# Optimization experiments

Hardware: AMD Instinct MI355X
Metric: run time of the kernel (lower is better)

Reference implementation:

```python
import jax, jax.numpy as jnp
import numpy as np

BS, H, L, D = 16, 16, 4096, 32  # bs, n_heads, seq_len(=q_len), head_dim

def setup_inputs() -> dict:
    key = jax.random.key(0)
    kq, kk, kv = jax.random.split(key, 3)
    q = jax.random.normal(kq, (BS, H, L, D), dtype=jnp.float32)
    k = jax.random.normal(kk, (BS, H, D, L), dtype=jnp.float32)
    v = jax.random.normal(kv, (BS, H, L, D), dtype=jnp.float32)
    return {"q": q, "k": k, "v": v}

def reference(q, k, v):
    # reordered attention: scores = (k @ v) / sqrt(seq_len) -> [bs,h,d_k,d_v]
    seq_len = v.shape[2]
    scores = jnp.einsum('bhds,bhse->bhde', k, v) / jnp.sqrt(jnp.float32(seq_len))
    # faithful to source: softmax over dim=0 (the batch dimension)
    attn_weights = jax.nn.softmax(scores, axis=0)
    # dropout p=0.0 -> identity
    # output = q @ weights -> [bs,h,q_len,d_v]
    output = jnp.einsum('bhld,bhde->bhle', q, attn_weights)
    return output, attn_weights
```

## Files before the change

### kernel.cpp

```cpp
#include <hip/hip_runtime.h>

#define BS 16
#define NH 16
#define LQ 4096
#define DH 32

constexpr int SPLIT = 8;
constexpr int SCHUNK = LQ / SPLIT;
constexpr size_t OUT_ELEMS = (size_t)BS * NH * LQ * DH;
constexpr int HDE = NH * DH * DH;

__device__ __forceinline__ void async_cp16(float* dst, const float* src) {
    __builtin_amdgcn_global_load_lds(
        (const __attribute__((address_space(1))) void*)src,
        (__attribute__((address_space(3))) void*)dst, 16, 0, 0);
}

__device__ __forceinline__ void fma4(float4& a, float s, const float4& v) {
    a.x = fmaf(s, v.x, a.x);
    a.y = fmaf(s, v.y, a.y);
    a.z = fmaf(s, v.z, a.z);
    a.w = fmaf(s, v.w, a.w);
}

__global__ __launch_bounds__(256, 2) void kv_partial(const float* __restrict__ k,
                                                     const float* __restrict__ v,
                                                     float* __restrict__ part) {
    __shared__ float lds[16384];
    const int tid  = threadIdx.x;
    const int wid  = tid >> 6;
    const int lane = tid & 63;
    const int p    = blockIdx.x & (SPLIT - 1);
    const int bh   = blockIdx.x >> 3;

    const int dgl = lane >> 3;
    const int d0  = dgl << 2;
    const int e0  = (lane & 7) << 2;

    const float* kb = k + (size_t)bh * DH * LQ;
    const float* vb = v + (size_t)bh * LQ * DH;
    const int s_blk = p * SCHUNK;

    float* kt = lds;
    float* vt = lds + 8192;

    float4 acc0 = {0,0,0,0}, acc1 = {0,0,0,0}, acc2 = {0,0,0,0}, acc3 = {0,0,0,0};

#pragma unroll
    for (int st = 0; st < 2; ++st) {
        const int sb = s_blk + (st << 8);

#pragma unroll
        for (int i = 0; i < 8; ++i) {
            const int d = (wid << 3) + i;
            async_cp16(kt + (d << 8),
                       kb + (size_t)d * LQ + sb + ((lane ^ (d >> 2)) << 2));
            const int o = (((wid << 3) + i) << 8);
            async_cp16(vt + o, vb + (((size_t)sb) << 5) + o + (lane << 2));
        }
        __syncthreads();

#pragma unroll 4
        for (int gg = 0; gg < 16; ++gg) {
            const int g  = (wid << 4) + gg;
            const int ko = (g ^ dgl) << 2;
            const float4 kq0 = *(const float4*)(kt + ((d0 + 0) << 8) + ko);
            const float4 kq1 = *(const float4*)(kt + ((d0 + 1) << 8) + ko);
            const float4 kq2 = *(const float4*)(kt + ((d0 + 2) << 8) + ko);
            const float4 kq3 = *(const float4*)(kt + ((d0 + 3) << 8) + ko);
            const int vo = (g << 7) + e0;
            const float4 vv0 = *(const float4*)(vt + vo);
            const float4 vv1 = *(const float4*)(vt + vo + 32);
            const float4 vv2 = *(const float4*)(vt + vo + 64);
            const float4 vv3 = *(const float4*)(vt + vo + 96);

            fma4(acc0, kq0.x, vv0); fma4(acc0, kq0.y, vv1); fma4(acc0, kq0.z, vv2); fma4(acc0, kq0.w, vv3);
            fma4(acc1, kq1.x, vv0); fma4(acc1, kq1.y, vv1); fma4(acc1, kq1.z, vv2); fma4(acc1, kq1.w, vv3);
            fma4(acc2, kq2.x, vv0); fma4(acc2, kq2.y, vv1); fma4(acc2, kq2.z, vv2); fma4(acc2, kq2.w, vv3);
            fma4(acc3, kq3.x, vv0); fma4(acc3, kq3.y, vv1); fma4(acc3, kq3.z, vv2); fma4(acc3, kq3.w, vv3);
        }
        __syncthreads();
    }

    float* red = lds;
    *(float4*)(red + (wid << 10) + ((d0 + 0) << 5) + e0) = acc0;
    *(float4*)(red + (wid << 10) + ((d0 + 1) << 5) + e0) = acc1;
    *(float4*)(red + (wid << 10) + ((d0 + 2) << 5) + e0) = acc2;
    *(float4*)(red + (wid << 10) + ((d0 + 3) << 5) + e0) = acc3;
    __syncthreads();

    const int t4 = tid << 2;
    const float4 r0 = *(const float4*)(red + t4);
    const float4 r1 = *(const float4*)(red + 1024 + t4);
    const float4 r2 = *(const float4*)(red + 2048 + t4);
    const float4 r3 = *(const float4*)(red + 3072 + t4);
    float4 r;
    r.x = (r0.x + r1.x) + (r2.x + r3.x);
    r.y = (r0.y + r1.y) + (r2.y + r3.y);
    r.z = (r0.z + r1.z) + (r2.z + r3.z);
    r.w = (r0.w + r1.w) + (r2.w + r3.w);
    *(float4*)(part + ((size_t)p * (BS * NH) + bh) * 1024 + t4) = r;
}

__global__ __launch_bounds__(256) void softmax_b(const float* __restrict__ part,
                                                 float* __restrict__ wts) {
    int idx = blockIdx.x * 256 + threadIdx.x;

    float sc[BS];
#pragma unroll
    for (int b = 0; b < BS; ++b) {
        float s = 0.f;
#pragma unroll
        for (int pp = 0; pp < SPLIT; ++pp) {
            s += part[(((size_t)pp * BS * NH + (size_t)b * NH) << 10) + idx];
        }
        sc[b] = s * (1.0f / 64.0f);
    }

    float m = sc[0];
#pragma unroll
    for (int b = 1; b < BS; ++b) m = fmaxf(m, sc[b]);
    float sum = 0.f;
#pragma unroll
    for (int b = 0; b < BS; ++b) { sc[b] = __expf(sc[b] - m); sum += sc[b]; }
    float inv = 1.0f / sum;
#pragma unroll
    for (int b = 0; b < BS; ++b) {
        wts[(size_t)b * HDE + idx] = sc[b] * inv;
    }
}

__global__ __launch_bounds__(256, 2) void qw(const float* __restrict__ q,
                                             const float* __restrict__ wts,
                                             float* __restrict__ out) {
    __shared__ float qs[128 * 36];
    const int blk = blockIdx.x;
    const int bh  = blk >> 5;
    const int lt  = blk & 31;
    const int tid = threadIdx.x;

    const float* qbase = q + ((size_t)bh * LQ + lt * 128) * DH;

#pragma unroll
    for (int pp = 0; pp < 4; ++pp) {
        const int idx = pp * 256 + tid;
        const int row = idx >> 3;
        const int c4  = idx & 7;
        const float4 t = *(const float4*)(qbase + idx * 4);
        *(float4*)(qs + row * 36 + c4 * 4) = t;
    }

    const int lsub = tid >> 3;
    const int e0   = (tid & 7) << 2;

    float4 Wf[32];
    const float* wbase = wts + (size_t)bh * (DH * DH) + e0;
#pragma unroll
    for (int d = 0; d < 32; ++d) Wf[d] = *(const float4*)(wbase + d * DH);

    __syncthreads();

    float* obase = out + ((size_t)bh * LQ + lt * 128) * DH;

#pragma unroll
    for (int r = 0; r < 4; ++r) {
        const int lr = lsub + r * 32;
        const float* qrow = qs + lr * 36;
        float4 acc = {0,0,0,0};
#pragma unroll
        for (int d4 = 0; d4 < 32; d4 += 4) {
            const float4 qv = *(const float4*)(qrow + d4);
            fma4(acc, qv.x, Wf[d4 + 0]);
            fma4(acc, qv.y, Wf[d4 + 1]);
            fma4(acc, qv.z, Wf[d4 + 2]);
            fma4(acc, qv.w, Wf[d4 + 3]);
        }
        *(float4*)(obase + (size_t)lr * DH + e0) = acc;
    }
}

extern "C" void kernel_launch(void* const* d_in, const int* in_sizes, int n_in,
                              void* d_out, int out_size, void* d_ws, size_t ws_size,
                              hipStream_t stream) {
    const float* q = (const float*)d_in[0];
    const float* k = (const float*)d_in[1];
    const float* v = (const float*)d_in[2];
    float* out  = (float*)d_out;
    float* wts  = out + OUT_ELEMS;
    float* part = (float*)d_ws;

    kv_partial<<<BS * NH * SPLIT, 256, 0, stream>>>(k, v, part);
    softmax_b<<<HDE / 256, 256, 0, stream>>>(part, wts);
    qw<<<BS * NH * (LQ / 128), 256, 0, stream>>>(q, wts, out);
}
```

Measured before the change: 160.2 us.

## Make kv_partial waves independent with register-prefetched double buffering in private LDS

Each wave of kv_partial now owns a private LDS slice and a contiguous 128-element sequence range. It prefetches K and V tiles into registers while computing on the current tile, which replaces the block-wide async global-to-LDS copies and __syncthreads barriers. LDS use is halved and launch bounds are raised to four blocks per CU to increase occupancy. The risks are higher register pressure, and correctness now relies on wave-local ordering enforced with s_waitcnt instead of barriers.

Measured after the change: 217.0 us. 35.4% more time.

```diff
diff --git a/kernel.cpp b/kernel.cpp
--- a/kernel.cpp
+++ b/kernel.cpp
@@ -9,12 +9,6 @@
 constexpr int SCHUNK = LQ / SPLIT;
 constexpr size_t OUT_ELEMS = (size_t)BS * NH * LQ * DH;
 constexpr int HDE = NH * DH * DH;
-
-__device__ __forceinline__ void async_cp16(float* dst, const float* src) {
-    __builtin_amdgcn_global_load_lds(
-        (const __attribute__((address_space(1))) void*)src,
-        (__attribute__((address_space(3))) void*)dst, 16, 0, 0);
-}
 
 __device__ __forceinline__ void fma4(float4& a, float s, const float4& v) {
     a.x = fmaf(s, v.x, a.x);
@@ -23,10 +17,10 @@
     a.w = fmaf(s, v.w, a.w);
 }
 
-__global__ __launch_bounds__(256, 2) void kv_partial(const float* __restrict__ k,
+__global__ __launch_bounds__(256, 4) void kv_partial(const float* __restrict__ k,
                                                      const float* __restrict__ v,
                                                      float* __restrict__ part) {
-    __shared__ float lds[16384];
+    __shared__ float lds[8192];
     const int tid  = threadIdx.x;
     const int wid  = tid >> 6;
     const int lane = tid & 63;
@@ -39,61 +33,76 @@
 
     const float* kb = k + (size_t)bh * DH * LQ;
     const float* vb = v + (size_t)bh * LQ * DH;
-    const int s_blk = p * SCHUNK;
-
-    float* kt = lds;
-    float* vt = lds + 8192;
+    const int s_wave = p * SCHUNK + (wid << 7);
+
+    float* kw = lds + (wid << 11);
+    float* vw = kw + 1024;
+
+    const int kd = lane >> 1;
+    const float* kg = kb + (size_t)kd * LQ + s_wave + ((lane & 1) << 4);
+    const float* vg = vb + ((size_t)s_wave << 5) + (lane << 2);
+
+    int kst[4];
+#pragma unroll
+    for (int j = 0; j < 4; ++j)
+        kst[j] = (kd << 5) + ((((((lane & 1) << 2) | j) ^ (kd >> 2)) & 7) << 2);
+
+    float4 kr[4], vr[4];
+#pragma unroll
+    for (int j = 0; j < 4; ++j) kr[j] = *(const float4*)(kg + (j << 2));
+#pragma unroll
+    for (int i = 0; i < 4; ++i) vr[i] = *(const float4*)(vg + (i << 8));
 
     float4 acc0 = {0,0,0,0}, acc1 = {0,0,0,0}, acc2 = {0,0,0,0}, acc3 = {0,0,0,0};
 
-#pragma unroll
-    for (int st = 0; st < 2; ++st) {
-        const int sb = s_blk + (st << 8);
-
-#pragma unroll
-        for (int i = 0; i < 8; ++i) {
-            const int d = (wid << 3) + i;
-            async_cp16(kt + (d << 8),
-                       kb + (size_t)d * LQ + sb + ((lane ^ (d >> 2)) << 2));
-            const int o = (((wid << 3) + i) << 8);
-            async_cp16(vt + o, vb + (((size_t)sb) << 5) + o + (lane << 2));
-        }
-        __syncthreads();
-
-#pragma unroll 4
-        for (int gg = 0; gg < 16; ++gg) {
-            const int g  = (wid << 4) + gg;
-            const int ko = (g ^ dgl) << 2;
-            const float4 kq0 = *(const float4*)(kt + ((d0 + 0) << 8) + ko);
-            const float4 kq1 = *(const float4*)(kt + ((d0 + 1) << 8) + ko);
-            const float4 kq2 = *(const float4*)(kt + ((d0 + 2) << 8) + ko);
-            const float4 kq3 = *(const float4*)(kt + ((d0 + 3) << 8) + ko);
+#pragma unroll 1
+    for (int t = 0; t < 4; ++t) {
+        asm volatile("s_waitcnt lgkmcnt(0)" ::: "memory");
+#pragma unroll
+        for (int j = 0; j < 4; ++j) *(float4*)(kw + kst[j]) = kr[j];
+#pragma unroll
+        for (int i = 0; i < 4; ++i) *(float4*)(vw + (i << 8) + (lane << 2)) = vr[i];
+
+        if (t < 3) {
+            const int so = (t + 1) << 5;
+#pragma unroll
+            for (int j = 0; j < 4; ++j) kr[j] = *(const float4*)(kg + so + (j << 2));
+#pragma unroll
+            for (int i = 0; i < 4; ++i) vr[i] = *(const float4*)(vg + ((size_t)so << 5) + (i << 8));
+        }
+
+#pragma unroll
+        for (int g = 0; g < 8; ++g) {
+            const int ko = (d0 << 5) + ((g ^ dgl) << 2);
+            const float4 kq0 = *(const float4*)(kw + ko);
+            const float4 kq1 = *(const float4*)(kw + ko + 32);
+            const float4 kq2 = *(const float4*)(kw + ko + 64);
+            const float4 kq3 = *(const float4*)(kw + ko + 96);
             const int vo = (g << 7) + e0;
-            const float4 vv0 = *(const float4*)(vt + vo);
-            const float4 vv1 = *(const float4*)(vt + vo + 32);
-            const float4 vv2 = *(const float4*)(vt + vo + 64);
-            const float4 vv3 = *(const float4*)(vt + vo + 96);
+            const float4 vv0 = *(const float4*)(vw + vo);
+            const float4 vv1 = *(const float4*)(vw + vo + 32);
+            const float4 vv2 = *(const float4*)(vw + vo + 64);
+            const float4 vv3 = *(const float4*)(vw + vo + 96);
 
             fma4(acc0, kq0.x, vv0); fma4(acc0, kq0.y, vv1); fma4(acc0, kq0.z, vv2); fma4(acc0, kq0.w, vv3);
             fma4(acc1, kq1.x, vv0); fma4(acc1, kq1.y, vv1); fma4(acc1, kq1.z, vv2); fma4(acc1, kq1.w, vv3);
             fma4(acc2, kq2.x, vv0); fma4(acc2, kq2.y, vv1); fma4(acc2, kq2.z, vv2); fma4(acc2, kq2.w, vv3);
             fma4(acc3, kq3.x, vv0); fma4(acc3, kq3.y, vv1); fma4(acc3, kq3.z, vv2); fma4(acc3, kq3.w, vv3);
         }
-        __syncthreads();
-    }
-
-    float* red = lds;
-    *(float4*)(red + (wid << 10) + ((d0 + 0) << 5) + e0) = acc0;
-    *(float4*)(red + (wid << 10) + ((d0 + 1) << 5) + e0) = acc1;
-    *(float4*)(red + (wid << 10) + ((d0 + 2) << 5) + e0) = acc2;
-    *(float4*)(red + (wid << 10) + ((d0 + 3) << 5) + e0) = acc3;
+    }
+
+    asm volatile("s_waitcnt lgkmcnt(0)" ::: "memory");
+    *(float4*)(kw + ((d0 + 0) << 5) + e0) = acc0;
+    *(float4*)(kw + ((d0 + 1) << 5) + e0) = acc1;
+    *(float4*)(kw + ((d0 + 2) << 5) + e0) = acc2;
+    *(float4*)(kw + ((d0 + 3) << 5) + e0) = acc3;
     __syncthreads();
 
     const int t4 = tid << 2;
-    const float4 r0 = *(const float4*)(red + t4);
-    const float4 r1 = *(const float4*)(red + 1024 + t4);
-    const float4 r2 = *(const float4*)(red + 2048 + t4);
-    const float4 r3 = *(const float4*)(red + 3072 + t4);
+    const float4 r0 = *(const float4*)(lds + t4);
+    const float4 r1 = *(const float4*)(lds + 2048 + t4);
+    const float4 r2 = *(const float4*)(lds + 4096 + t4);
+    const float4 r3 = *(const float4*)(lds + 6144 + t4);
     float4 r;
     r.x = (r0.x + r1.x) + (r2.x + r3.x);
     r.y = (r0.y + r1.y) + (r2.y + r3.y);
```

## Split KV reduction into finer sequence chunks with separate partial-sum reduce kernel

Applied to the files above, without the earlier changes.

The K·V partial kernel now works on 128-wide sequence chunks with half the LDS and a higher occupancy hint. When the workspace is large enough it launches 32 splits per (b,h) instead of 8, which raises the block count. The partial sums are reduced in a new fully parallel kernel that writes scaled scores into the weights buffer, and the softmax then runs in place. The cost is more partial-sum traffic and one extra kernel launch.

Result: faster. 146.0 us (-8.9%).

```diff
diff --git a/kernel.cpp b/kernel.cpp
--- a/kernel.cpp
+++ b/kernel.cpp
@@ -5,8 +5,6 @@
 #define LQ 4096
 #define DH 32
 
-constexpr int SPLIT = 8;
-constexpr int SCHUNK = LQ / SPLIT;
 constexpr size_t OUT_ELEMS = (size_t)BS * NH * LQ * DH;
 constexpr int HDE = NH * DH * DH;
 
@@ -23,15 +21,17 @@
     a.w = fmaf(s, v.w, a.w);
 }
 
-__global__ __launch_bounds__(256, 2) void kv_partial(const float* __restrict__ k,
+template<int NCH>
+__global__ __launch_bounds__(256, 5) void kv_partial(const float* __restrict__ k,
                                                      const float* __restrict__ v,
                                                      float* __restrict__ part) {
-    __shared__ float lds[16384];
+    __shared__ float lds[8192];
     const int tid  = threadIdx.x;
     const int wid  = tid >> 6;
     const int lane = tid & 63;
-    const int p    = blockIdx.x & (SPLIT - 1);
-    const int bh   = blockIdx.x >> 3;
+    const int nsplit = 32 / NCH;
+    const int p  = blockIdx.x % nsplit;
+    const int bh = blockIdx.x / nsplit;
 
     const int dgl = lane >> 3;
     const int d0  = dgl << 2;
@@ -39,35 +39,42 @@
 
     const float* kb = k + (size_t)bh * DH * LQ;
     const float* vb = v + (size_t)bh * LQ * DH;
-    const int s_blk = p * SCHUNK;
-
     float* kt = lds;
-    float* vt = lds + 8192;
+    float* vt = lds + 4096;
+
+    size_t ksrc[4];
+    int kdst[4];
+    size_t vsrc[4];
+#pragma unroll
+    for (int i = 0; i < 4; ++i) {
+        const int j = (wid << 2) + i;
+        const int d = (j << 1) + (lane >> 5);
+        const int gs = lane & 31;
+        const int gsrc = (gs & 24) | ((gs ^ ((j >> 1) & 7)) & 7);
+        ksrc[i] = (size_t)d * LQ + (gsrc << 2);
+        kdst[i] = j << 8;
+        vsrc[i] = (size_t)(j << 8) + (lane << 2);
+    }
 
     float4 acc0 = {0,0,0,0}, acc1 = {0,0,0,0}, acc2 = {0,0,0,0}, acc3 = {0,0,0,0};
 
 #pragma unroll
-    for (int st = 0; st < 2; ++st) {
-        const int sb = s_blk + (st << 8);
-
-#pragma unroll
-        for (int i = 0; i < 8; ++i) {
-            const int d = (wid << 3) + i;
-            async_cp16(kt + (d << 8),
-                       kb + (size_t)d * LQ + sb + ((lane ^ (d >> 2)) << 2));
-            const int o = (((wid << 3) + i) << 8);
-            async_cp16(vt + o, vb + (((size_t)sb) << 5) + o + (lane << 2));
-        }
+    for (int c = 0; c < NCH; ++c) {
+        const int s0 = (p * NCH + c) << 7;
+#pragma unroll
+        for (int i = 0; i < 4; ++i) async_cp16(kt + kdst[i], kb + ksrc[i] + s0);
+#pragma unroll
+        for (int i = 0; i < 4; ++i) async_cp16(vt + kdst[i], vb + ((size_t)s0 << 5) + vsrc[i]);
         __syncthreads();
 
-#pragma unroll 4
-        for (int gg = 0; gg < 16; ++gg) {
-            const int g  = (wid << 4) + gg;
-            const int ko = (g ^ dgl) << 2;
-            const float4 kq0 = *(const float4*)(kt + ((d0 + 0) << 8) + ko);
-            const float4 kq1 = *(const float4*)(kt + ((d0 + 1) << 8) + ko);
-            const float4 kq2 = *(const float4*)(kt + ((d0 + 2) << 8) + ko);
-            const float4 kq3 = *(const float4*)(kt + ((d0 + 3) << 8) + ko);
+#pragma unroll
+        for (int gg = 0; gg < 8; ++gg) {
+            const int g  = (wid << 3) + gg;
+            const int ko = ((g & 24) | ((g ^ dgl) & 7)) << 2;
+            const float4 kq0 = *(const float4*)(kt + ((d0 + 0) << 7) + ko);
+            const float4 kq1 = *(const float4*)(kt + ((d0 + 1) << 7) + ko);
+            const float4 kq2 = *(const float4*)(kt + ((d0 + 2) << 7) + ko);
+            const float4 kq3 = *(const float4*)(kt + ((d0 + 3) << 7) + ko);
             const int vo = (g << 7) + e0;
             const float4 vv0 = *(const float4*)(vt + vo);
             const float4 vv1 = *(const float4*)(vt + vo + 32);
@@ -82,18 +89,17 @@
         __syncthreads();
     }
 
-    float* red = lds;
-    *(float4*)(red + (wid << 10) + ((d0 + 0) << 5) + e0) = acc0;
-    *(float4*)(red + (wid << 10) + ((d0 + 1) << 5) + e0) = acc1;
-    *(float4*)(red + (wid << 10) + ((d0 + 2) << 5) + e0) = acc2;
-    *(float4*)(red + (wid << 10) + ((d0 + 3) << 5) + e0) = acc3;
+    *(float4*)(lds + (wid << 10) + ((d0 + 0) << 5) + e0) = acc0;
+    *(float4*)(lds + (wid << 10) + ((d0 + 1) << 5) + e0) = acc1;
+    *(float4*)(lds + (wid << 10) + ((d0 + 2) << 5) + e0) = acc2;
+    *(float4*)(lds + (wid << 10) + ((d0 + 3) << 5) + e0) = acc3;
     __syncthreads();
 
     const int t4 = tid << 2;
-    const float4 r0 = *(const float4*)(red + t4);
-    const float4 r1 = *(const float4*)(red + 1024 + t4);
-    const float4 r2 = *(const float4*)(red + 2048 + t4);
-    const float4 r3 = *(const float4*)(red + 3072 + t4);
+    const float4 r0 = *(const float4*)(lds + t4);
+    const float4 r1 = *(const float4*)(lds + 1024 + t4);
+    const float4 r2 = *(const float4*)(lds + 2048 + t4);
+    const float4 r3 = *(const float4*)(lds + 3072 + t4);
     float4 r;
     r.x = (r0.x + r1.x) + (r2.x + r3.x);
     r.y = (r0.y + r1.y) + (r2.y + r3.y);
@@ -102,21 +108,23 @@
     *(float4*)(part + ((size_t)p * (BS * NH) + bh) * 1024 + t4) = r;
 }
 
-__global__ __launch_bounds__(256) void softmax_b(const float* __restrict__ part,
-                                                 float* __restrict__ wts) {
-    int idx = blockIdx.x * 256 + threadIdx.x;
+__global__ __launch_bounds__(256) void reduce_p(const float* __restrict__ part,
+                                                float* __restrict__ scores, int nsp) {
+    const int gidx = blockIdx.x * 256 + threadIdx.x;
+    const int b    = gidx >> 14;
+    const int idx  = gidx & 16383;
+    float s = 0.f;
+    for (int pp = 0; pp < nsp; ++pp)
+        s += part[((size_t)pp << 18) + ((size_t)b << 14) + idx];
+    scores[gidx] = s * (1.0f / 64.0f);
+}
+
+__global__ __launch_bounds__(256) void softmax_b(float* __restrict__ wts) {
+    const int idx = blockIdx.x * 256 + threadIdx.x;
 
     float sc[BS];
 #pragma unroll
-    for (int b = 0; b < BS; ++b) {
-        float s = 0.f;
-#pragma unroll
-        for (int pp = 0; pp < SPLIT; ++pp) {
-            s += part[(((size_t)pp * BS * NH + (size_t)b * NH) << 10) + idx];
-        }
-        sc[b] = s * (1.0f / 64.0f);
-    }
-
+    for (int b = 0; b < BS; ++b) sc[b] = wts[((size_t)b << 14) + idx];
     float m = sc[0];
 #pragma unroll
     for (int b = 1; b < BS; ++b) m = fmaxf(m, sc[b]);
@@ -125,9 +133,7 @@
     for (int b = 0; b < BS; ++b) { sc[b] = __expf(sc[b] - m); sum += sc[b]; }
     float inv = 1.0f / sum;
 #pragma unroll
-    for (int b = 0; b < BS; ++b) {
-        wts[(size_t)b * HDE + idx] = sc[b] * inv;
-    }
+    for (int b = 0; b < BS; ++b) wts[((size_t)b << 14) + idx] = sc[b] * inv;
 }
 
 __global__ __launch_bounds__(256, 2) void qw(const float* __restrict__ q,
@@ -153,8 +159,9 @@
     const int lsub = tid >> 3;
     const int e0   = (tid & 7) << 2;
 
+    const int b = bh >> 4, h = bh & 15;
     float4 Wf[32];
-    const float* wbase = wts + (size_t)bh * (DH * DH) + e0;
+    const float* wbase = wts + ((size_t)b << 14) + ((size_t)h << 10) + e0;
 #pragma unroll
     for (int d = 0; d < 32; ++d) Wf[d] = *(const float4*)(wbase + d * DH);
 
@@ -189,7 +196,16 @@
     float* wts  = out + OUT_ELEMS;
     float* part = (float*)d_ws;
 
-    kv_partial<<<BS * NH * SPLIT, 256, 0, stream>>>(k, v, part);
-    softmax_b<<<HDE / 256, 256, 0, stream>>>(part, wts);
+    const size_t need32 = (size_t)32 * 256 * 1024 * 4;
+    int nsp;
+    if (ws_size >= need32) {
+        kv_partial<1><<<256 * 32, 256, 0, stream>>>(k, v, part);
+        nsp = 32;
+    } else {
+        kv_partial<4><<<256 * 8, 256, 0, stream>>>(k, v, part);
+        nsp = 8;
+    }
+    reduce_p<<<(BS * HDE) / 256, 256, 0, stream>>>(part, wts, nsp);
+    softmax_b<<<HDE / 256, 256, 0, stream>>>(wts);
     qw<<<BS * NH * (LQ / 128), 256, 0, stream>>>(q, wts, out);
 }
```

## Compute K·V partials from registers with split-S threads and LDS tree reduction

Applied to the files above, without the earlier changes.

The kv_partial kernel no longer stages K and V tiles in LDS through async global-to-LDS copies. Each thread now loads its K (8 d-rows) and V (8 e-columns) slices straight into registers with software double-buffering, computes an 8x8 outer-product tile over 32 s-values, and combines the 16 s-groups with a log-step tree reduction in LDS. The aim is to remove LDS traffic and staging barriers from the main loop and give each thread more register reuse. In exchange the kernel uses many more registers and adds eight barrier phases in the reduction. The softmax kernel is renamed, its index math switched to shifts, and qw's weight addressing is rewritten equivalently.

Result: slower. 262.4 us (+63.8%).

```diff
diff --git a/kernel.cpp b/kernel.cpp
--- a/kernel.cpp
+++ b/kernel.cpp
@@ -6,15 +6,8 @@
 #define DH 32
 
 constexpr int SPLIT = 8;
-constexpr int SCHUNK = LQ / SPLIT;
 constexpr size_t OUT_ELEMS = (size_t)BS * NH * LQ * DH;
 constexpr int HDE = NH * DH * DH;
-
-__device__ __forceinline__ void async_cp16(float* dst, const float* src) {
-    __builtin_amdgcn_global_load_lds(
-        (const __attribute__((address_space(1))) void*)src,
-        (__attribute__((address_space(3))) void*)dst, 16, 0, 0);
-}
 
 __device__ __forceinline__ void fma4(float4& a, float s, const float4& v) {
     a.x = fmaf(s, v.x, a.x);
@@ -23,97 +16,120 @@
     a.w = fmaf(s, v.w, a.w);
 }
 
+__device__ __forceinline__ void add4(float4& a, const float4& b) {
+    a.x += b.x; a.y += b.y; a.z += b.z; a.w += b.w;
+}
+
 __global__ __launch_bounds__(256, 2) void kv_partial(const float* __restrict__ k,
                                                      const float* __restrict__ v,
                                                      float* __restrict__ part) {
-    __shared__ float lds[16384];
-    const int tid  = threadIdx.x;
-    const int wid  = tid >> 6;
-    const int lane = tid & 63;
-    const int p    = blockIdx.x & (SPLIT - 1);
-    const int bh   = blockIdx.x >> 3;
-
-    const int dgl = lane >> 3;
-    const int d0  = dgl << 2;
-    const int e0  = (lane & 7) << 2;
-
-    const float* kb = k + (size_t)bh * DH * LQ;
-    const float* vb = v + (size_t)bh * LQ * DH;
-    const int s_blk = p * SCHUNK;
-
-    float* kt = lds;
-    float* vt = lds + 8192;
-
-    float4 acc0 = {0,0,0,0}, acc1 = {0,0,0,0}, acc2 = {0,0,0,0}, acc3 = {0,0,0,0};
-
-#pragma unroll
-    for (int st = 0; st < 2; ++st) {
-        const int sb = s_blk + (st << 8);
-
+    __shared__ float red[8192];
+    const int tid = threadIdx.x;
+    const int p   = blockIdx.x & (SPLIT - 1);
+    const int bh  = blockIdx.x >> 3;
+    const int sp  = tid >> 4;
+    const int tw  = tid & 15;
+    const int d0  = ((tw >> 2) & 3) << 3;
+    const int e0  = (tw & 3) << 3;
+
+    const float* kptr = k + (size_t)bh * DH * LQ + (size_t)d0 * LQ + p * 512 + sp * 32;
+    const float* vptr = v + (size_t)bh * LQ * DH + (size_t)(p * 512 + sp * 32) * DH + e0;
+
+    float4 acc[8][2];
+#pragma unroll
+    for (int i = 0; i < 8; ++i) {
+        acc[i][0] = make_float4(0.f, 0.f, 0.f, 0.f);
+        acc[i][1] = make_float4(0.f, 0.f, 0.f, 0.f);
+    }
+
+    float4 kq[2][8], vv[2][8];
+#pragma unroll
+    for (int i = 0; i < 8; ++i) kq[0][i] = *(const float4*)(kptr + (size_t)i * LQ);
+#pragma unroll
+    for (int si = 0; si < 4; ++si) {
+        vv[0][si * 2 + 0] = *(const float4*)(vptr + si * DH);
+        vv[0][si * 2 + 1] = *(const float4*)(vptr + si * DH + 4);
+    }
+
+#pragma unroll
+    for (int ss = 0; ss < 8; ++ss) {
+        const int cur = ss & 1, nxt = cur ^ 1;
+        if (ss < 7) {
+            const int sof = (ss + 1) << 2;
+#pragma unroll
+            for (int i = 0; i < 8; ++i)
+                kq[nxt][i] = *(const float4*)(kptr + (size_t)i * LQ + sof);
+#pragma unroll
+            for (int si = 0; si < 4; ++si) {
+                vv[nxt][si * 2 + 0] = *(const float4*)(vptr + (sof + si) * DH);
+                vv[nxt][si * 2 + 1] = *(const float4*)(vptr + (sof + si) * DH + 4);
+            }
+        }
+#pragma unroll
+        for (int si = 0; si < 4; ++si) {
+            const float4 v0 = vv[cur][si * 2], v1 = vv[cur][si * 2 + 1];
+#pragma unroll
+            for (int i = 0; i < 8; ++i) {
+                const float ks = (si == 0) ? kq[cur][i].x
+                               : (si == 1) ? kq[cur][i].y
+                               : (si == 2) ? kq[cur][i].z : kq[cur][i].w;
+                fma4(acc[i][0], ks, v0);
+                fma4(acc[i][1], ks, v1);
+            }
+        }
+    }
+
+#pragma unroll
+    for (int step = 8; step >= 1; step >>= 1) {
+        if (sp >= step && sp < 2 * step) {
+            float* dst = red + (((sp - step) << 4) + tw) * 64;
+#pragma unroll
+            for (int i = 0; i < 8; ++i) {
+                *(float4*)(dst + i * 8)     = acc[i][0];
+                *(float4*)(dst + i * 8 + 4) = acc[i][1];
+            }
+        }
+        __syncthreads();
+        if (sp < step) {
+            const float* src = red + ((sp << 4) + tw) * 64;
+#pragma unroll
+            for (int i = 0; i < 8; ++i) {
+                add4(acc[i][0], *(const float4*)(src + i * 8));
+                add4(acc[i][1], *(const float4*)(src + i * 8 + 4));
+            }
+        }
+        __syncthreads();
+    }
+
+    if (sp == 0) {
+        float* dst = red + tw * 64;
 #pragma unroll
         for (int i = 0; i < 8; ++i) {
-            const int d = (wid << 3) + i;
-            async_cp16(kt + (d << 8),
-                       kb + (size_t)d * LQ + sb + ((lane ^ (d >> 2)) << 2));
-            const int o = (((wid << 3) + i) << 8);
-            async_cp16(vt + o, vb + (((size_t)sb) << 5) + o + (lane << 2));
-        }
-        __syncthreads();
-
-#pragma unroll 4
-        for (int gg = 0; gg < 16; ++gg) {
-            const int g  = (wid << 4) + gg;
-            const int ko = (g ^ dgl) << 2;
-            const float4 kq0 = *(const float4*)(kt + ((d0 + 0) << 8) + ko);
-            const float4 kq1 = *(const float4*)(kt + ((d0 + 1) << 8) + ko);
-            const float4 kq2 = *(const float4*)(kt + ((d0 + 2) << 8) + ko);
-            const float4 kq3 = *(const float4*)(kt + ((d0 + 3) << 8) + ko);
-            const int vo = (g << 7) + e0;
-            const float4 vv0 = *(const float4*)(vt + vo);
-            const float4 vv1 = *(const float4*)(vt + vo + 32);
-            const float4 vv2 = *(const float4*)(vt + vo + 64);
-            const float4 vv3 = *(const float4*)(vt + vo + 96);
-
-            fma4(acc0, kq0.x, vv0); fma4(acc0, kq0.y, vv1); fma4(acc0, kq0.z, vv2); fma4(acc0, kq0.w, vv3);
-            fma4(acc1, kq1.x, vv0); fma4(acc1, kq1.y, vv1); fma4(acc1, kq1.z, vv2); fma4(acc1, kq1.w, vv3);
-            fma4(acc2, kq2.x, vv0); fma4(acc2, kq2.y, vv1); fma4(acc2, kq2.z, vv2); fma4(acc2, kq2.w, vv3);
-            fma4(acc3, kq3.x, vv0); fma4(acc3, kq3.y, vv1); fma4(acc3, kq3.z, vv2); fma4(acc3, kq3.w, vv3);
-        }
-        __syncthreads();
-    }
-
-    float* red = lds;
-    *(float4*)(red + (wid << 10) + ((d0 + 0) << 5) + e0) = acc0;
-    *(float4*)(red + (wid << 10) + ((d0 + 1) << 5) + e0) = acc1;
-    *(float4*)(red + (wid << 10) + ((d0 + 2) << 5) + e0) = acc2;
-    *(float4*)(red + (wid << 10) + ((d0 + 3) << 5) + e0) = acc3;
+            *(float4*)(dst + i * 8)     = acc[i][0];
+            *(float4*)(dst + i * 8 + 4) = acc[i][1];
+        }
+    }
     __syncthreads();
 
-    const int t4 = tid << 2;
-    const float4 r0 = *(const float4*)(red + t4);
-    const float4 r1 = *(const float4*)(red + 1024 + t4);
-    const float4 r2 = *(const float4*)(red + 2048 + t4);
-    const float4 r3 = *(const float4*)(red + 3072 + t4);
-    float4 r;
-    r.x = (r0.x + r1.x) + (r2.x + r3.x);
-    r.y = (r0.y + r1.y) + (r2.y + r3.y);
-    r.z = (r0.z + r1.z) + (r2.z + r3.z);
-    r.w = (r0.w + r1.w) + (r2.w + r3.w);
-    *(float4*)(part + ((size_t)p * (BS * NH) + bh) * 1024 + t4) = r;
-}
-
-__global__ __launch_bounds__(256) void softmax_b(const float* __restrict__ part,
-                                                 float* __restrict__ wts) {
-    int idx = blockIdx.x * 256 + threadIdx.x;
+    const int d   = tid >> 3;
+    const int e4  = (tid & 7) << 2;
+    const int tws = ((d >> 3) << 2) | (e4 >> 3);
+    const int src = tws * 64 + (d & 7) * 8 + (e4 & 7);
+    *(float4*)(part + ((size_t)p * (BS * NH) + bh) * 1024 + (tid << 2)) =
+        *(const float4*)(red + src);
+}
+
+__global__ __launch_bounds__(256) void finalize_w(const float* __restrict__ part,
+                                                  float* __restrict__ wts) {
+    const int idx = blockIdx.x * 256 + threadIdx.x;
 
     float sc[BS];
 #pragma unroll
     for (int b = 0; b < BS; ++b) {
         float s = 0.f;
 #pragma unroll
-        for (int pp = 0; pp < SPLIT; ++pp) {
-            s += part[(((size_t)pp * BS * NH + (size_t)b * NH) << 10) + idx];
-        }
+        for (int pp = 0; pp < SPLIT; ++pp)
+            s += part[((size_t)pp << 18) + ((size_t)b << 14) + idx];
         sc[b] = s * (1.0f / 64.0f);
     }
 
@@ -123,11 +139,9 @@
     float sum = 0.f;
 #pragma unroll
     for (int b = 0; b < BS; ++b) { sc[b] = __expf(sc[b] - m); sum += sc[b]; }
-    float inv = 1.0f / sum;
-#pragma unroll
-    for (int b = 0; b < BS; ++b) {
-        wts[(size_t)b * HDE + idx] = sc[b] * inv;
-    }
+    const float inv = 1.0f / sum;
+#pragma unroll
+    for (int b = 0; b < BS; ++b) wts[((size_t)b << 14) + idx] = sc[b] * inv;
 }
 
 __global__ __launch_bounds__(256, 2) void qw(const float* __restrict__ q,
@@ -153,8 +167,9 @@
     const int lsub = tid >> 3;
     const int e0   = (tid & 7) << 2;
 
+    const int b = bh >> 4, h = bh & 15;
     float4 Wf[32];
-    const float* wbase = wts + (size_t)bh * (DH * DH) + e0;
+    const float* wbase = wts + ((size_t)b << 14) + ((size_t)h << 10) + e0;
 #pragma unroll
     for (int d = 0; d < 32; ++d) Wf[d] = *(const float4*)(wbase + d * DH);
 
@@ -166,7 +181,7 @@
     for (int r = 0; r < 4; ++r) {
         const int lr = lsub + r * 32;
         const float* qrow = qs + lr * 36;
-        float4 acc = {0,0,0,0};
+        float4 acc = {0, 0, 0, 0};
 #pragma unroll
         for (int d4 = 0; d4 < 32; d4 += 4) {
             const float4 qv = *(const float4*)(qrow + d4);
@@ -190,6 +205,6 @@
     float* part = (float*)d_ws;
 
     kv_partial<<<BS * NH * SPLIT, 256, 0, stream>>>(k, v, part);
-    softmax_b<<<HDE / 256, 256, 0, stream>>>(part, wts);
+    finalize_w<<<HDE / 256, 256, 0, stream>>>(part, wts);
     qw<<<BS * NH * (LQ / 128), 256, 0, stream>>>(q, wts, out);
 }
```
